# Performance work log

Hardware: AMD Instinct MI355X
Metric: run time of the kernel (lower is better)

Reference implementation:

```python
import jax, jax.numpy as jnp
import numpy as np

NUM_CONTEXT = 8  # context panels; +1 choice -> 9 panels, 72 ordered pairs (i != j)

_PAIRS = np.array([(i, j) for i in range(9) for j in range(9) if i != j], dtype=np.int32)
I_IDX = jnp.asarray(_PAIRS[:, 0])  # [72]
J_IDX = jnp.asarray(_PAIRS[:, 1])  # [72]


def setup_inputs() -> dict:
    key = jax.random.key(0)
    ks = jax.random.split(key, 10)
    B, C, F, H = 256, 8, 512, 256
    s_in = 1.0 / np.sqrt(2 * F)
    s_h = 1.0 / np.sqrt(H)
    return {
        "context_features": jax.random.normal(ks[0], (B, NUM_CONTEXT, F), jnp.float32),
        "choice_features": jax.random.normal(ks[1], (B, C, F), jnp.float32),
        "W1": jax.random.uniform(ks[2], (2 * F, H), jnp.float32, -s_in, s_in),
        "b1": jax.random.uniform(ks[3], (H,), jnp.float32, -s_in, s_in),
        "W2": jax.random.uniform(ks[4], (H, H), jnp.float32, -s_h, s_h),
        "b2": jax.random.uniform(ks[5], (H,), jnp.float32, -s_h, s_h),
        "W3": jax.random.uniform(ks[6], (H, H), jnp.float32, -s_h, s_h),
        "b3": jax.random.uniform(ks[7], (H,), jnp.float32, -s_h, s_h),
        "W4": jax.random.uniform(ks[8], (H, 1), jnp.float32, -s_h, s_h),
        "b4": jax.random.uniform(ks[9], (1,), jnp.float32, -s_h, s_h),
    }


def reference(context_features, choice_features, W1, b1, W2, b2, W3, b3, W4, b4):
    B, C, F = choice_features.shape[0], choice_features.shape[1], choice_features.shape[2]
    # panels[b, c, p, f]: 8 context panels + 1 choice panel per candidate choice
    ctx = jnp.broadcast_to(context_features[:, None, :, :], (B, C, NUM_CONTEXT, F))
    panels = jnp.concatenate([ctx, choice_features[:, :, None, :]], axis=2)  # [B,C,9,F]
    # all 72 ordered pairs (i != j), concatenated features -> [B,C,72,2F]
    pair = jnp.concatenate([panels[:, :, I_IDX, :], panels[:, :, J_IDX, :]], axis=-1)
    # g_theta MLP
    h = jax.nn.relu(pair @ W1 + b1)
    h = jax.nn.relu(h @ W2 + b2)        # [B,C,72,H]
    agg = h.mean(axis=2)                # [B,C,H]
    # f_phi MLP (dropout is identity in eval mode)
    g = jax.nn.relu(agg @ W3 + b3)
    score = g @ W4 + b4                 # [B,C,1]
    return score[..., 0]                # [B,C]
```

## Files before the change

kernel.cpp:

```cpp
#include <hip/hip_runtime.h>
#include <hip/hip_bf16.h>


typedef __bf16 bf16_t;
typedef bf16_t bf16x8 __attribute__((ext_vector_type(8)));
typedef bf16_t bf16x4 __attribute__((ext_vector_type(4)));
typedef float f32x4 __attribute__((ext_vector_type(4)));

#define MFMA16(a, b, c) __builtin_amdgcn_mfma_f32_16x16x32_bf16((a), (b), (c), 0, 0, 0)

__global__ __launch_bounds__(256) void prep_kernel(
    const float* __restrict__ ctx, const float* __restrict__ cho,
    const float* __restrict__ W1, const float* __restrict__ W2,
    const float* __restrict__ W3, bf16_t* __restrict__ Xb,
    bf16_t* __restrict__ Wp, bf16_t* __restrict__ W2T,
    bf16_t* __restrict__ W3T) {
  const int blk = blockIdx.x;
  const int t = threadIdx.x;
  if (blk < 2048) {
    const int row = blk * 2 + (t >> 7);
    const int c4 = (t & 127) * 4;
    const int bi = row >> 4;
    const int p = row & 15;
    const float* src = (p < 8) ? ctx + (size_t)(bi * 8 + p) * 512 + c4
                               : cho + (size_t)(bi * 8 + (p - 8)) * 512 + c4;
    const f32x4 x = *(const f32x4*)src;
    bf16x4 y;
    for (int e = 0; e < 4; ++e) y[e] = (bf16_t)x[e];
    *(bf16x4*)(Xb + (size_t)row * 512 + c4) = y;
  } else {
    const int idx = (blk - 2048) * 256 + t;
    if (idx < 262144) {
      const int j = idx >> 9, k = idx & 511;
      const float v = (j < 256) ? W1[k * 256 + j] : W1[(512 + k) * 256 + (j - 256)];
      Wp[idx] = (bf16_t)v;
    } else if (idx < 327680) {
      const int s = idx - 262144;
      const int n = s >> 8, k = s & 255;
      W2T[s] = (bf16_t)W2[k * 256 + n];
    } else {
      const int s = idx - 327680;
      const int n = s >> 8, k = s & 255;
      W3T[s] = (bf16_t)W3[k * 256 + n];
    }
  }
}

__global__ __launch_bounds__(256) void k1_kernel(
    const bf16_t* __restrict__ Xb, const bf16_t* __restrict__ Wp,
    float* __restrict__ UV) {
  const int bm = blockIdx.x & 63;
  const int bn = blockIdx.x >> 6;
  const int t = threadIdx.x;
  const int lane = t & 63;
  const int w = t >> 6;
  const int col = lane & 15;
  const int quad = lane >> 4;
  const int n = bn * 64 + w * 16 + col;
  f32x4 acc[4] = {};
  for (int ks = 0; ks < 16; ++ks) {
    const int k = ks * 32 + quad * 8;
    bf16x8 af[4];
    for (int mt = 0; mt < 4; ++mt) {
      const int r = bm * 64 + mt * 16 + col;
      af[mt] = *(const bf16x8*)(Xb + (size_t)r * 512 + k);
    }
    const bf16x8 bf = *(const bf16x8*)(Wp + (size_t)n * 512 + k);
    for (int mt = 0; mt < 4; ++mt) acc[mt] = MFMA16(af[mt], bf, acc[mt]);
  }
  for (int mt = 0; mt < 4; ++mt)
    for (int reg = 0; reg < 4; ++reg) {
      const int r = bm * 64 + mt * 16 + quad * 4 + reg;
      UV[(size_t)r * 512 + n] = acc[mt][reg];
    }
}

__global__ __launch_bounds__(512) void k2_kernel(
    const float* __restrict__ UV, const float* __restrict__ b1,
    const float* __restrict__ b2, const bf16_t* __restrict__ W2T,
    const bf16_t* __restrict__ W3T, const float* __restrict__ b3,
    const float* __restrict__ W4, const float* __restrict__ b4,
    float* __restrict__ out) {
  __shared__ char smem[52224];
  bf16_t (*h1)[136] = (bf16_t(*)[136])smem;
  float (*S)[256] = (float(*)[256])smem;
  bf16_t (*Ag)[264] = (bf16_t(*)[264])(smem + 9216);
  float (*red)[8] = (float(*)[8])(smem + 9216 + 8448);
  const int b = blockIdx.x;
  const int t = threadIdx.x;
  const int lane = t & 63;
  const int w = t >> 6;
  const int col = lane & 15;
  const int quad = lane >> 4;
  const float* su = nullptr;
  const float* sv = nullptr;
  int sr = 0, sc0 = 0;
  if (t < 384) {
    sr = t >> 1;
    sc0 = (t & 1) * 64;
    if (sr < 56) {
      const int i = sr / 7;
      const int jj = sr - i * 7;
      const int j = jj + (jj >= i ? 1 : 0);
      su = UV + (size_t)(b * 16 + i) * 512;
      sv = UV + (size_t)(b * 16 + j) * 512 + 256;
    } else if (sr >= 64) {
      const int ch = (sr - 64) >> 4;
      const int rr = (sr - 64) & 15;
      if (rr < 8) {
        su = UV + (size_t)(b * 16 + 8 + ch) * 512;
        sv = UV + (size_t)(b * 16 + rr) * 512 + 256;
      } else {
        su = UV + (size_t)(b * 16 + (rr - 8)) * 512;
        sv = UV + (size_t)(b * 16 + 8 + ch) * 512 + 256;
      }
    }
  }
  const int mtb = (w & 1) * 6;
  const int q = w >> 1;
  f32x4 acc[6][4] = {};
  for (int half = 0; half < 2; ++half) {
    const int kbase = half * 128;
    if (t < 384) {
      if (su) {
        for (int c = sc0; c < sc0 + 64; c += 4) {
          const f32x4 uu = *(const f32x4*)(su + kbase + c);
          const f32x4 vv = *(const f32x4*)(sv + kbase + c);
          const f32x4 bb = *(const f32x4*)(b1 + kbase + c);
          bf16x4 y;
          for (int e = 0; e < 4; ++e) y[e] = (bf16_t)fmaxf(uu[e] + vv[e] + bb[e], 0.0f);
          *(bf16x4*)(&h1[sr][c]) = y;
        }
      } else {
        for (int c = sc0; c < sc0 + 64; c += 4)
          *(bf16x4*)(&h1[sr][c]) = (bf16x4)0.0f;
      }
    }
    __syncthreads();
    for (int ks = 0; ks < 4; ++ks) {
      const int k = ks * 32 + quad * 8;
      bf16x8 af[6], bf[4];
      for (int mt = 0; mt < 6; ++mt)
        af[mt] = *(const bf16x8*)(&h1[(mtb + mt) * 16 + col][k]);
      for (int nt = 0; nt < 4; ++nt) {
        const int n = q * 64 + nt * 16 + col;
        bf[nt] = *(const bf16x8*)(W2T + (size_t)n * 256 + kbase + k);
      }
      for (int mt = 0; mt < 6; ++mt)
        for (int nt = 0; nt < 4; ++nt)
          acc[mt][nt] = MFMA16(af[mt], bf[nt], acc[mt][nt]);
    }
    __syncthreads();
  }
  for (int nt = 0; nt < 4; ++nt) {
    const int n = q * 64 + nt * 16 + col;
    const float b2c = b2[n];
    float sctx = 0.0f;
    for (int mt = 0; mt < 6; ++mt) {
      const int gm = mtb + mt;
      float s = 0.0f;
      for (int reg = 0; reg < 4; ++reg) {
        const int row = gm * 16 + quad * 4 + reg;
        if (row < 56 || row >= 64) s += fmaxf(acc[mt][nt][reg] + b2c, 0.0f);
      }
      s += __shfl_xor(s, 16);
      s += __shfl_xor(s, 32);
      if (gm < 4) {
        sctx += s;
      } else if (lane < 16) {
        S[1 + (gm - 4)][n] = s;
      }
    }
    if (mtb == 0 && lane < 16) S[0][n] = sctx;
  }
  __syncthreads();
  {
    const int ch = t >> 6;
    const int n0 = (t & 63) * 4;
    bf16x4 y;
    for (int e = 0; e < 4; ++e)
      y[e] = (bf16_t)((S[0][n0 + e] + S[1 + ch][n0 + e]) * (1.0f / 72.0f));
    *(bf16x4*)(&Ag[ch][n0]) = y;
    *(bf16x4*)(&Ag[8 + ch][n0]) = (bf16x4)0.0f;
  }
  __syncthreads();
  f32x4 acc2[2] = {};
  for (int ks = 0; ks < 8; ++ks) {
    const int k = ks * 32 + quad * 8;
    const bf16x8 af = *(const bf16x8*)(&Ag[col][k]);
    for (int nt = 0; nt < 2; ++nt) {
      const int n = w * 32 + nt * 16 + col;
      const bf16x8 bf = *(const bf16x8*)(W3T + (size_t)n * 256 + k);
      acc2[nt] = MFMA16(af, bf, acc2[nt]);
    }
  }
  for (int reg = 0; reg < 4; ++reg) {
    float pr = 0.0f;
    for (int nt = 0; nt < 2; ++nt) {
      const int n = w * 32 + nt * 16 + col;
      pr += fmaxf(acc2[nt][reg] + b3[n], 0.0f) * W4[n];
    }
    pr += __shfl_xor(pr, 1);
    pr += __shfl_xor(pr, 2);
    pr += __shfl_xor(pr, 4);
    pr += __shfl_xor(pr, 8);
    if (col == 0 && quad < 2) red[w][quad * 4 + reg] = pr;
  }
  __syncthreads();
  if (t < 8) {
    float sc = b4[0];
    for (int ww = 0; ww < 8; ++ww) sc += red[ww][t];
    out[b * 8 + t] = sc;
  }
}

extern "C" void kernel_launch(void* const* d_in, const int* in_sizes, int n_in,
                              void* d_out, int out_size, void* d_ws, size_t ws_size,
                              hipStream_t stream) {
  (void)in_sizes; (void)n_in; (void)out_size; (void)ws_size;
  const float* ctx = (const float*)d_in[0];
  const float* cho = (const float*)d_in[1];
  const float* W1  = (const float*)d_in[2];
  const float* b1  = (const float*)d_in[3];
  const float* W2  = (const float*)d_in[4];
  const float* b2  = (const float*)d_in[5];
  const float* W3  = (const float*)d_in[6];
  const float* b3  = (const float*)d_in[7];
  const float* W4  = (const float*)d_in[8];
  const float* b4  = (const float*)d_in[9];
  char* ws = (char*)d_ws;
  bf16_t* Wp   = (bf16_t*)(ws + 0);
  bf16_t* W2T  = (bf16_t*)(ws + 524288);
  bf16_t* W3T  = (bf16_t*)(ws + 655360);
  bf16_t* Xb   = (bf16_t*)(ws + 786432);
  float*  UV   = (float*)(ws + 4980736);
  float*  out  = (float*)d_out;

  prep_kernel<<<dim3(3584), dim3(256), 0, stream>>>(ctx, cho, W1, W2, W3, Xb, Wp, W2T, W3T);
  k1_kernel<<<dim3(512), dim3(256), 0, stream>>>(Xb, Wp, UV);
  k2_kernel<<<dim3(256), dim3(512), 0, stream>>>(UV, b1, b2, W2T, W3T, b3, W4, b4, out);
}
```

Measured before the change: 129.5 us.

## Fuse fp32-to-bf16 input conversion into first GEMM via LDS staging

Result: faster. 115.7 us (-10.7%).

```diff
diff --git a/kernel.cpp b/kernel.cpp
--- a/kernel.cpp
+++ b/kernel.cpp
@@ -10,45 +10,29 @@
 #define MFMA16(a, b, c) __builtin_amdgcn_mfma_f32_16x16x32_bf16((a), (b), (c), 0, 0, 0)
 
 __global__ __launch_bounds__(256) void prep_kernel(
+    const float* __restrict__ W1, const float* __restrict__ W2,
+    const float* __restrict__ W3, bf16_t* __restrict__ Wp,
+    bf16_t* __restrict__ W2T, bf16_t* __restrict__ W3T) {
+  const int idx = blockIdx.x * 256 + threadIdx.x;
+  if (idx < 262144) {
+    const int j = idx >> 9, k = idx & 511;
+    const float v = (j < 256) ? W1[k * 256 + j] : W1[(512 + k) * 256 + (j - 256)];
+    Wp[idx] = (bf16_t)v;
+  } else if (idx < 327680) {
+    const int s = idx - 262144;
+    const int n = s >> 8, k = s & 255;
+    W2T[s] = (bf16_t)W2[k * 256 + n];
+  } else {
+    const int s = idx - 327680;
+    const int n = s >> 8, k = s & 255;
+    W3T[s] = (bf16_t)W3[k * 256 + n];
+  }
+}
+
+__global__ __launch_bounds__(256) void k1_kernel(
     const float* __restrict__ ctx, const float* __restrict__ cho,
-    const float* __restrict__ W1, const float* __restrict__ W2,
-    const float* __restrict__ W3, bf16_t* __restrict__ Xb,
-    bf16_t* __restrict__ Wp, bf16_t* __restrict__ W2T,
-    bf16_t* __restrict__ W3T) {
-  const int blk = blockIdx.x;
-  const int t = threadIdx.x;
-  if (blk < 2048) {
-    const int row = blk * 2 + (t >> 7);
-    const int c4 = (t & 127) * 4;
-    const int bi = row >> 4;
-    const int p = row & 15;
-    const float* src = (p < 8) ? ctx + (size_t)(bi * 8 + p) * 512 + c4
-                               : cho + (size_t)(bi * 8 + (p - 8)) * 512 + c4;
-    const f32x4 x = *(const f32x4*)src;
-    bf16x4 y;
-    for (int e = 0; e < 4; ++e) y[e] = (bf16_t)x[e];
-    *(bf16x4*)(Xb + (size_t)row * 512 + c4) = y;
-  } else {
-    const int idx = (blk - 2048) * 256 + t;
-    if (idx < 262144) {
-      const int j = idx >> 9, k = idx & 511;
-      const float v = (j < 256) ? W1[k * 256 + j] : W1[(512 + k) * 256 + (j - 256)];
-      Wp[idx] = (bf16_t)v;
-    } else if (idx < 327680) {
-      const int s = idx - 262144;
-      const int n = s >> 8, k = s & 255;
-      W2T[s] = (bf16_t)W2[k * 256 + n];
-    } else {
-      const int s = idx - 327680;
-      const int n = s >> 8, k = s & 255;
-      W3T[s] = (bf16_t)W3[k * 256 + n];
-    }
-  }
-}
-
-__global__ __launch_bounds__(256) void k1_kernel(
-    const bf16_t* __restrict__ Xb, const bf16_t* __restrict__ Wp,
-    float* __restrict__ UV) {
+    const bf16_t* __restrict__ Wp, float* __restrict__ UV) {
+  __shared__ bf16_t As[64][264];
   const int bm = blockIdx.x & 63;
   const int bn = blockIdx.x >> 6;
   const int t = threadIdx.x;
@@ -57,16 +41,33 @@
   const int col = lane & 15;
   const int quad = lane >> 4;
   const int n = bn * 64 + w * 16 + col;
+  const int sr = t >> 2;
+  const int gr = bm * 64 + sr;
+  const int bi = gr >> 4;
+  const int p = gr & 15;
+  const float* src = (p < 8) ? ctx + (size_t)(bi * 8 + p) * 512
+                             : cho + (size_t)(bi * 8 + (p - 8)) * 512;
+  const int cb = (t & 3) * 4;
   f32x4 acc[4] = {};
-  for (int ks = 0; ks < 16; ++ks) {
-    const int k = ks * 32 + quad * 8;
-    bf16x8 af[4];
-    for (int mt = 0; mt < 4; ++mt) {
-      const int r = bm * 64 + mt * 16 + col;
-      af[mt] = *(const bf16x8*)(Xb + (size_t)r * 512 + k);
-    }
-    const bf16x8 bf = *(const bf16x8*)(Wp + (size_t)n * 512 + k);
-    for (int mt = 0; mt < 4; ++mt) acc[mt] = MFMA16(af[mt], bf, acc[mt]);
+  for (int half = 0; half < 2; ++half) {
+    const int kbase = half * 256;
+    for (int i = 0; i < 16; ++i) {
+      const int c = cb + i * 16;
+      const f32x4 x = *(const f32x4*)(src + kbase + c);
+      bf16x4 y;
+      for (int e = 0; e < 4; ++e) y[e] = (bf16_t)x[e];
+      *(bf16x4*)(&As[sr][c]) = y;
+    }
+    __syncthreads();
+    for (int ks = 0; ks < 8; ++ks) {
+      const int k = ks * 32 + quad * 8;
+      bf16x8 af[4];
+      for (int mt = 0; mt < 4; ++mt)
+        af[mt] = *(const bf16x8*)(&As[mt * 16 + col][k]);
+      const bf16x8 bf = *(const bf16x8*)(Wp + (size_t)n * 512 + kbase + k);
+      for (int mt = 0; mt < 4; ++mt) acc[mt] = MFMA16(af[mt], bf, acc[mt]);
+    }
+    __syncthreads();
   }
   for (int mt = 0; mt < 4; ++mt)
     for (int reg = 0; reg < 4; ++reg) {
@@ -232,11 +233,10 @@
   bf16_t* Wp   = (bf16_t*)(ws + 0);
   bf16_t* W2T  = (bf16_t*)(ws + 524288);
   bf16_t* W3T  = (bf16_t*)(ws + 655360);
-  bf16_t* Xb   = (bf16_t*)(ws + 786432);
-  float*  UV   = (float*)(ws + 4980736);
+  float*  UV   = (float*)(ws + 786432);
   float*  out  = (float*)d_out;
 
-  prep_kernel<<<dim3(3584), dim3(256), 0, stream>>>(ctx, cho, W1, W2, W3, Xb, Wp, W2T, W3T);
-  k1_kernel<<<dim3(512), dim3(256), 0, stream>>>(Xb, Wp, UV);
+  prep_kernel<<<dim3(1536), dim3(256), 0, stream>>>(W1, W2, W3, Wp, W2T, W3T);
+  k1_kernel<<<dim3(512), dim3(256), 0, stream>>>(ctx, cho, Wp, UV);
   k2_kernel<<<dim3(256), dim3(512), 0, stream>>>(UV, b1, b2, W2T, W3T, b3, W4, b4, out);
 }
```
